# Performance work log

Measured on AMD Instinct MI355X. Metric: run time of the kernel, lower is better.

Reference implementation:

```python
import jax, jax.numpy as jnp
import numpy as np

NUM_NODES = 50000
NUM_RELATIONS = 16
HIDDEN = 128
NUM_LAYERS = 3
NUM_EDGES = 1600000


def setup_inputs() -> dict:
    key = jax.random.key(0)
    ks = jax.random.split(key, 6)
    edge_index = jax.random.randint(ks[0], (2, NUM_EDGES), 0, NUM_NODES, dtype=jnp.int64)
    edge_type = jax.random.randint(ks[1], (NUM_EDGES,), 0, NUM_RELATIONS, dtype=jnp.int64)
    scale = 1.0 / np.sqrt(HIDDEN)
    node_init = jax.random.normal(ks[2], (NUM_NODES, HIDDEN), dtype=jnp.float32) * scale
    W = jax.random.normal(ks[3], (NUM_LAYERS, NUM_RELATIONS, HIDDEN, HIDDEN), dtype=jnp.float32) * scale
    root = jax.random.normal(ks[4], (NUM_LAYERS, HIDDEN, HIDDEN), dtype=jnp.float32) * scale
    bias = jnp.zeros((NUM_LAYERS, HIDDEN), dtype=jnp.float32)
    return {"edge_index": edge_index, "edge_type": edge_type,
            "node_init": node_init, "W": W, "root": root, "bias": bias}


def _fast_rgcn_layer(x, src, tgt, edge_type, W_r, root_r, bias_r):
    # FastRGCNConv with aggr='mean': mean of messages per (target node, relation),
    # message = x_src @ W[relation]. By linearity, aggregate normalized x_src per
    # (node, relation) first, then apply relation weights with a single einsum.
    N, d = x.shape
    R = W_r.shape[0]
    seg = tgt * R + edge_type                       # combined (node, relation) segment id
    msg = x[src]                                    # [E, d] irregular gather
    agg = jax.ops.segment_sum(msg, seg, num_segments=N * R).reshape(N, R, d)
    cnt = jax.ops.segment_sum(jnp.ones_like(edge_type, dtype=x.dtype), seg,
                              num_segments=N * R).reshape(N, R, 1)
    agg = agg / jnp.clip(cnt, 1.0, None)            # per-(node,relation) mean
    out = jnp.einsum('nrd,rdo->no', agg, W_r)       # relation-specific transform
    out = out + x @ root_r + bias_r                 # root/self connection + bias
    return out


def reference(edge_index, edge_type, node_init, W, root, bias):
    src, tgt = edge_index[0], edge_index[1]
    x = node_init
    for i in range(NUM_LAYERS):
        x = _fast_rgcn_layer(x, src, tgt, edge_type, W[i], root[i], bias[i])
        if i < NUM_LAYERS - 1:
            x = jax.nn.relu(x)  # dropout omitted (eval mode)
    return x
```

## Files before the change

### kernel.cpp

```cpp
#include <hip/hip_runtime.h>
#include <hip/hip_bf16.h>

#define N_NODES   50000
#define N_REL     16
#define HID       128
#define N_EDGES   1600000
#define N_TILES   3125
#define N_BINS    800000
#define N_RUNS    50000
#define N_SCANBLK 49
#define N_MBLK    1563
#define PAYLOAD_CAP 2400064
#define BS_LAYER  278528
#define AG_STRIDE 136

typedef unsigned short ushort_t;
typedef __attribute__((ext_vector_type(8))) short short8;
typedef __attribute__((ext_vector_type(4))) float f32x4;

union BF2U { __hip_bfloat162 h; unsigned u; };

__device__ __forceinline__ unsigned pack_bf16_2(float x, float y) {
  BF2U c; c.h = __float22bfloat162_rn(make_float2(x, y));
  return c.u;
}

__device__ __forceinline__ void lds_barrier() {
  asm volatile("s_waitcnt lgkmcnt(0)\n\ts_barrier" ::: "memory");
}


__global__ __launch_bounds__(256) void k_hist(const int* __restrict__ ei,
                                              const int* __restrict__ et,
                                              int* __restrict__ cnt,
                                              int* __restrict__ rank) {
  int e = blockIdx.x * 256 + threadIdx.x;
  int tgt = ei[N_EDGES + e];
  int r   = et[e];
  int key = ((tgt >> 4) << 8) | (r << 4) | (tgt & 15);
  rank[e] = atomicAdd(&cnt[key], 1);
}

__global__ __launch_bounds__(1024) void k_runpad_btot(const int* __restrict__ cnt,
                                                      int* __restrict__ run_start,
                                                      int* __restrict__ totals) {
  __shared__ int s[1024];
  int t = threadIdx.x, blk = blockIdx.x;
  int r = blk * 1024 + t;
  int v = 0;
  if (r < N_RUNS) {
    const int4* c4 = (const int4*)(cnt + r * 16);
    int sum = 0;
#pragma unroll
    for (int j = 0; j < 4; ++j) { int4 w = c4[j]; sum += w.x + w.y + w.z + w.w; }
    v = (sum + 15) & ~15;
    run_start[r] = v;
  }
  s[t] = v; __syncthreads();
  for (int ofs = 512; ofs > 0; ofs >>= 1) {
    if (t < ofs) s[t] += s[t + ofs];
    __syncthreads();
  }
  if (t == 0) totals[blk] = s[0];
}

__global__ __launch_bounds__(1024) void k_scan_totals(int* totals, int* endp, int nblk) {
  __shared__ int s[1024];
  int t = threadIdx.x;
  int v = (t < nblk) ? totals[t] : 0;
  s[t] = v; __syncthreads();
  for (int ofs = 1; ofs < 1024; ofs <<= 1) {
    int x = (t >= ofs) ? s[t - ofs] : 0;
    __syncthreads();
    s[t] += x;
    __syncthreads();
  }
  if (t < nblk) totals[t] = s[t] - v;
  if (t == nblk - 1) *endp = s[t];
}

__global__ __launch_bounds__(1024) void k_scan_fineoff(int* __restrict__ run_start,
                                                       const int* __restrict__ totals,
                                                       const int* __restrict__ cnt,
                                                       int* __restrict__ fine_start,
                                                       unsigned* __restrict__ payload) {
  __shared__ int s[1024];
  int t = threadIdx.x, blk = blockIdx.x;
  int r = blk * 1024 + t;
  int v = (r < N_RUNS) ? run_start[r] : 0;
  s[t] = v; __syncthreads();
  for (int ofs = 1; ofs < 1024; ofs <<= 1) {
    int x = (t >= ofs) ? s[t - ofs] : 0;
    __syncthreads();
    s[t] += x;
    __syncthreads();
  }
  if (r < N_RUNS) {
    int base = totals[blk] + s[t] - v;
    run_start[r] = base;
    int pfx = 0;
#pragma unroll 4
    for (int i = 0; i < 16; ++i) {
      fine_start[r * 16 + i] = base + pfx;
      pfx += cnt[r * 16 + i];
    }
    const unsigned dummy = ((unsigned)N_NODES << 16) | (1u << 4) | 15u;
    for (int j = base + pfx; j < base + v; ++j) payload[j] = dummy;
  }
}

__global__ __launch_bounds__(256) void k_sort(const int* __restrict__ ei,
                                              const int* __restrict__ et,
                                              const int* __restrict__ cnt,
                                              const int* __restrict__ fine_start,
                                              const int* __restrict__ rank,
                                              unsigned* __restrict__ payload) {
  int e = blockIdx.x * 256 + threadIdx.x;
  int src = ei[e];
  int tgt = ei[N_EDGES + e];
  int r   = et[e];
  int key = ((tgt >> 4) << 8) | (r << 4) | (tgt & 15);
  int c = cnt[key]; c = c > 4095 ? 4095 : c;
  int pos = fine_start[key] + rank[e];
  payload[pos] = ((unsigned)src << 16) | ((unsigned)c << 4) | (unsigned)(tgt & 15);
}

__global__ __launch_bounds__(256) void k_bt(const float* __restrict__ W,
                                            const float* __restrict__ root,
                                            ushort_t* __restrict__ Bs) {
  int idx = blockIdx.x * 256 + threadIdx.x;
  int lane = idx & 63;
  int fl   = idx >> 6;
  int frag = fl % 544;
  int l    = fl / 544;
  int cb = frag & 7, kk = (frag >> 3) & 3, r = frag >> 5;
  int col = cb * 16 + (lane & 15);
  int d0  = kk * 32 + (lane >> 4) * 8;
  const float* srcp = (r < 16)
      ? W + ((size_t)(l * N_REL + r) * HID + d0) * HID + col
      : root + ((size_t)l * HID + d0) * HID + col;
  ushort_t out[8];
#pragma unroll
  for (int j = 0; j < 8; ++j) {
    union { __hip_bfloat16 h; ushort_t u; } c;
    c.h = __float2bfloat16(srcp[(size_t)j * HID]);
    out[j] = c.u;
  }
  *(short8*)(Bs + ((size_t)fl << 9) + lane * 8) = *(short8*)out;
}

__global__ __launch_bounds__(256) void k_xh(const float* __restrict__ xin,
                                            ushort_t* __restrict__ xh_a,
                                            ushort_t* __restrict__ xh_b) {
  int i = blockIdx.x * 256 + threadIdx.x;
  float4 v = ((const float4*)xin)[i];
  uint2 u;
  u.x = pack_bf16_2(v.x, v.y);
  u.y = pack_bf16_2(v.z, v.w);
  ((uint2*)xh_a)[i] = u;
  if (blockIdx.x == 0 && threadIdx.x < 64) {
    uint2 z = {0u, 0u};
    ushort_t* dst = (threadIdx.x < 32) ? xh_a : xh_b;
    int k = threadIdx.x & 31;
    *(uint2*)(dst + (size_t)N_NODES * HID + k * 4) = z;
  }
}


__global__ __launch_bounds__(512, 8) void k_main(const ushort_t* __restrict__ xh,
                                                 ushort_t* __restrict__ xh_out,
                                                 float* __restrict__ fout,
                                                 const ushort_t* __restrict__ Bs,
                                                 const float* __restrict__ bias,
                                                 const int* __restrict__ run_start,
                                                 const unsigned* __restrict__ payload,
                                                 int write_f32) {
  __shared__ alignas(16) ushort_t agg[2][2][32][AG_STRIDE];

  const int tile0 = blockIdx.x * 2;
  const int tid   = threadIdx.x;
  const int wave  = tid >> 6;
  const int lane  = tid & 63;
  const int m16   = lane & 15;
  const int q     = lane >> 4;
  const unsigned* xh32 = (const unsigned*)xh;

  if (wave < 4) {
    const int p_rel  = wave & 1;
    const int p_tile = wave >> 1;
    const int rowb   = p_tile * 16;

    int ebv = 0;
    {
      int tt = tile0 + p_tile;
      int idx = (tt < N_TILES) ? (tt * 16 + (lane >> 1) * 2 + p_rel + (lane & 1))
                               : N_RUNS;
      if (lane < 16) ebv = run_start[idx];
    }

#define ISSUE16(DST, PV, JB)                                                  \
    _Pragma("unroll")                                                         \
    for (int k1 = 0; k1 < 16; ++k1) {                                         \
      unsigned spq = (unsigned)__builtin_amdgcn_readlane(PV, (JB) + k1);      \
      DST[k1] = xh32[(spq >> 16) * 64 + lane];                                \
    }

#define FLUSHM(BUF)                                                           \
    if (mcur >= 0) {                                                          \
      float sc = __builtin_amdgcn_rcpf((float)scnt);                          \
      *(unsigned*)&agg[BUF][p_rel][rowb + mcur][lane * 2] =                   \
          pack_bf16_2(a0 * sc, a1 * sc);                                      \
    }

#define CONSUME1(SPK, XV, BUF)                                                \
    {                                                                         \
      int mk = (int)((SPK) & 15u);                                            \
      if (mk != mcur) {                                                       \
        FLUSHM(BUF);                                                          \
        mcur = mk; scnt = (int)(((SPK) >> 4) & 4095u);                        \
        a0 = 0.f; a1 = 0.f;                                                   \
      }                                                                       \
      a0 += __uint_as_float((XV) << 16);                                      \
      a1 += __uint_as_float((XV) & 0xffff0000u);                              \
    }

#define CONS16(PV, JB, SLOT, BUF)                                             \
    _Pragma("unroll")                                                         \
    for (int k2 = 0; k2 < 16; ++k2) {                                         \
      unsigned spk = (unsigned)__builtin_amdgcn_readlane(PV, (JB) + k2);      \
      CONSUME1(spk, SLOT[k2], BUF);                                           \
    }

    unsigned xqA[16], xqB[16], xqE[16];

    int e0 = __builtin_amdgcn_readlane(ebv, 0);
    int e1 = __builtin_amdgcn_readlane(ebv, 1);
    int pv = (int)payload[e0 + lane];
    ISSUE16(xqA, pv, 0);

    for (int s = 0; s < 8; ++s) {
      const int buf = s & 1;
      int cnt = e1 - e0;

      if (cnt > 16) ISSUE16(xqB, pv, 16);
      if (cnt > 32) ISSUE16(xqE, pv, 32);

      int f0 = e0, f1 = e1, pvn = pv;
      if (s < 7) {
        f0 = __builtin_amdgcn_readlane(ebv, (s + 1) * 2);
        f1 = __builtin_amdgcn_readlane(ebv, (s + 1) * 2 + 1);
        pvn = (int)payload[f0 + lane];
      }

      {
        short8 z = {0, 0, 0, 0, 0, 0, 0, 0};
#pragma unroll
        for (int i = 0; i < 4; ++i)
          *(short8*)&agg[buf][p_rel][rowb + i * 4 + q][m16 * 8] = z;
      }

      {
        int mcur = -1, scnt = 1;
        float a0 = 0.f, a1 = 0.f;
        if (cnt > 0) {
          CONS16(pv, 0, xqA, buf);
          if (cnt > 16) {
            CONS16(pv, 16, xqB, buf);
            if (cnt > 32) {
              CONS16(pv, 32, xqE, buf);
              if (cnt > 48) {
                ISSUE16(xqB, pv, 48);
                CONS16(pv, 48, xqB, buf);
              }
            }
          }
          for (int c0 = e0 + 64; c0 < e1; c0 += 16) {
            int pvx = (int)payload[c0 + lane];
            ISSUE16(xqE, pvx, 0);
            CONS16(pvx, 0, xqE, buf);
          }
          FLUSHM(buf);
        }
      }

      if (s < 7) {
        e0 = f0; e1 = f1; pv = pvn;
        ISSUE16(xqA, pv, 0);
      }
      lds_barrier();
    }
#undef CONS16
#undef CONSUME1
#undef FLUSHM
#undef ISSUE16
    return;
  }

  const int cw = wave - 4;
  f32x4 acc[2][2];
#pragma unroll
  for (int t = 0; t < 2; ++t)
#pragma unroll
    for (int i = 0; i < 2; ++i) acc[t][i] = (f32x4){0.f, 0.f, 0.f, 0.f};

  for (int s = 0; s < 8; ++s) {
    lds_barrier();
#pragma unroll
    for (int rp = 0; rp < 2; ++rp) {
      int rel = s * 2 + rp;
      short8 Bf[4][2];
#pragma unroll
      for (int kk = 0; kk < 4; ++kk)
#pragma unroll
        for (int i = 0; i < 2; ++i)
          Bf[kk][i] = *(const short8*)(Bs +
              ((size_t)((rel * 4 + kk) * 8 + (cw * 2 + i)) << 9) + lane * 8);
#pragma unroll
      for (int kk = 0; kk < 4; ++kk) {
        short8 A0 = *(const short8*)&agg[s & 1][rp][m16][kk * 32 + q * 8];
        short8 A1 = *(const short8*)&agg[s & 1][rp][16 + m16][kk * 32 + q * 8];
#pragma unroll
        for (int i = 0; i < 2; ++i) {
          acc[0][i] = __builtin_amdgcn_mfma_f32_16x16x32_bf16(A0, Bf[kk][i], acc[0][i], 0, 0, 0);
          acc[1][i] = __builtin_amdgcn_mfma_f32_16x16x32_bf16(A1, Bf[kk][i], acc[1][i], 0, 0, 0);
        }
      }
    }
  }

  {
    short8 Bf[4][2];
#pragma unroll
    for (int kk = 0; kk < 4; ++kk)
#pragma unroll
      for (int i = 0; i < 2; ++i)
        Bf[kk][i] = *(const short8*)(Bs +
            ((size_t)((16 * 4 + kk) * 8 + (cw * 2 + i)) << 9) + lane * 8);
    int r0 = tile0 * 16 + m16;      if (r0 > N_NODES) r0 = N_NODES;
    int r1 = tile0 * 16 + 16 + m16; if (r1 > N_NODES) r1 = N_NODES;
#pragma unroll
    for (int kk = 0; kk < 4; ++kk) {
      short8 A0 = *(const short8*)(xh + (size_t)r0 * HID + kk * 32 + q * 8);
      short8 A1 = *(const short8*)(xh + (size_t)r1 * HID + kk * 32 + q * 8);
#pragma unroll
      for (int i = 0; i < 2; ++i) {
        acc[0][i] = __builtin_amdgcn_mfma_f32_16x16x32_bf16(A0, Bf[kk][i], acc[0][i], 0, 0, 0);
        acc[1][i] = __builtin_amdgcn_mfma_f32_16x16x32_bf16(A1, Bf[kk][i], acc[1][i], 0, 0, 0);
      }
    }
  }

  float bvv[2];
#pragma unroll
  for (int i = 0; i < 2; ++i) bvv[i] = bias[cw * 32 + i * 16 + m16];
  int rbase = tile0 * 16 + q * 4;
#pragma unroll
  for (int t = 0; t < 2; ++t)
#pragma unroll
    for (int rg = 0; rg < 4; ++rg) {
      int row = rbase + t * 16 + rg;
      if (row < N_NODES) {
#pragma unroll
        for (int i = 0; i < 2; ++i) {
          float v = acc[t][i][rg] + bvv[i];
          int col = cw * 32 + i * 16 + m16;
          if (write_f32) {
            fout[(size_t)row * HID + col] = v;
          } else {
            v = fmaxf(v, 0.f);
            union { __hip_bfloat16 h; ushort_t u; } cv;
            cv.h = __float2bfloat16(v);
            xh_out[(size_t)row * HID + col] = cv.u;
          }
        }
      }
    }
}


extern "C" void kernel_launch(void* const* d_in, const int* in_sizes, int n_in,
                              void* d_out, int out_size, void* d_ws, size_t ws_size,
                              hipStream_t stream) {
  const int*   ei        = (const int*)d_in[0];
  const int*   et        = (const int*)d_in[1];
  const float* node_init = (const float*)d_in[2];
  const float* W         = (const float*)d_in[3];
  const float* root      = (const float*)d_in[4];
  const float* bias      = (const float*)d_in[5];
  float* outp = (float*)d_out;

  char* ws = (char*)d_ws;
  size_t o = 0;
  auto carve = [&](size_t bytes) { char* p = ws + o; o = (o + bytes + 255) & ~(size_t)255; return p; };
  ushort_t* xh_a       = (ushort_t*)carve((size_t)(N_NODES + 1) * HID * 2);
  ushort_t* xh_b       = (ushort_t*)carve((size_t)(N_NODES + 1) * HID * 2);
  unsigned* payload    = (unsigned*)carve((size_t)PAYLOAD_CAP * 4);
  int*      cnt        = (int*)     carve((size_t)N_BINS * 4);
  int*      fine_start = (int*)     carve((size_t)N_BINS * 4);
  int*      rank       = (int*)     carve((size_t)N_EDGES * 4);
  int*      run_start  = (int*)     carve((size_t)(N_RUNS + 1) * 4);
  int*      totals     = (int*)     carve((size_t)N_SCANBLK * 4);
  ushort_t* Bs         = (ushort_t*)carve((size_t)3 * BS_LAYER * 2);
  (void)ws_size; (void)n_in; (void)in_sizes; (void)out_size;

  hipMemsetAsync(cnt, 0, (size_t)N_BINS * 4, stream);
  hipLaunchKernelGGL(k_hist,         dim3(N_EDGES / 256), dim3(256), 0, stream, ei, et, cnt, rank);
  hipLaunchKernelGGL(k_runpad_btot,  dim3(N_SCANBLK), dim3(1024), 0, stream, cnt, run_start, totals);
  hipLaunchKernelGGL(k_scan_totals,  dim3(1), dim3(1024), 0, stream, totals, run_start + N_RUNS, N_SCANBLK);
  hipLaunchKernelGGL(k_scan_fineoff, dim3(N_SCANBLK), dim3(1024), 0, stream, run_start, totals, cnt, fine_start, payload);
  hipLaunchKernelGGL(k_sort,         dim3(N_EDGES / 256), dim3(256), 0, stream, ei, et, cnt, fine_start, rank, payload);
  hipLaunchKernelGGL(k_bt,           dim3(3 * 544 * 64 / 256), dim3(256), 0, stream, W, root, Bs);
  hipLaunchKernelGGL(k_xh,           dim3(N_NODES * HID / 4 / 256), dim3(256), 0, stream, node_init, xh_a, xh_b);

  hipLaunchKernelGGL(k_main, dim3(N_MBLK), dim3(512), 0, stream,
                     xh_a, xh_b, (float*)nullptr,
                     Bs + (size_t)0 * BS_LAYER, bias + 0 * HID, run_start, payload, 0);
  hipLaunchKernelGGL(k_main, dim3(N_MBLK), dim3(512), 0, stream,
                     xh_b, xh_a, (float*)nullptr,
                     Bs + (size_t)1 * BS_LAYER, bias + 1 * HID, run_start, payload, 0);
  hipLaunchKernelGGL(k_main, dim3(N_MBLK), dim3(512), 0, stream,
                     xh_a, (ushort_t*)nullptr, outp,
                     Bs + (size_t)2 * BS_LAYER, bias + 2 * HID, run_start, payload, 1);
}
```

Baseline: 509.0 us.

## Collapse preprocessing kernels: single-pass scan with atomic cursor, packed key-rank, fused conversions

Replaces the three-kernel run/fine-offset scan with one kernel. Each block takes its base offset from an atomic cursor and stores a (base, count) pair per run, which the main kernel now reads. The histogram pass writes a packed key|rank word so the sort pass no longer re-reads target and edge-type arrays. The weight-transpose and feature bf16 conversion kernels are merged into one launch. The aim is fewer launches and serialization points plus less global traffic in preprocessing, at the cost of run placement order depending on block scheduling and an assumption that per-bin ranks fit in 12 bits.

```diff
diff --git a/kernel.cpp b/kernel.cpp
--- a/kernel.cpp
+++ b/kernel.cpp
@@ -13,6 +13,8 @@
 #define PAYLOAD_CAP 2400064
 #define BS_LAYER  278528
 #define AG_STRIDE 136
+#define XH_BLKS   6250
+#define BT_BLKS   408
 
 typedef unsigned short ushort_t;
 typedef __attribute__((ext_vector_type(8))) short short8;
@@ -33,41 +35,33 @@
 __global__ __launch_bounds__(256) void k_hist(const int* __restrict__ ei,
                                               const int* __restrict__ et,
                                               int* __restrict__ cnt,
-                                              int* __restrict__ rank) {
+                                              unsigned* __restrict__ keyrank) {
   int e = blockIdx.x * 256 + threadIdx.x;
   int tgt = ei[N_EDGES + e];
   int r   = et[e];
   int key = ((tgt >> 4) << 8) | (r << 4) | (tgt & 15);
-  rank[e] = atomicAdd(&cnt[key], 1);
-}
-
-__global__ __launch_bounds__(1024) void k_runpad_btot(const int* __restrict__ cnt,
-                                                      int* __restrict__ run_start,
-                                                      int* __restrict__ totals) {
+  int rk  = atomicAdd(&cnt[key], 1);
+  keyrank[e] = ((unsigned)key << 12) | (unsigned)rk;
+}
+
+__global__ __launch_bounds__(1024) void k_scanall(const int* __restrict__ cnt,
+                                                  int* __restrict__ run2,
+                                                  int* __restrict__ fine_start,
+                                                  unsigned* __restrict__ payload,
+                                                  int* __restrict__ cursor) {
   __shared__ int s[1024];
+  __shared__ int basesh;
   int t = threadIdx.x, blk = blockIdx.x;
   int r = blk * 1024 + t;
+  int4 c4[4];
   int v = 0;
   if (r < N_RUNS) {
-    const int4* c4 = (const int4*)(cnt + r * 16);
+    const int4* cp = (const int4*)(cnt + r * 16);
     int sum = 0;
 #pragma unroll
-    for (int j = 0; j < 4; ++j) { int4 w = c4[j]; sum += w.x + w.y + w.z + w.w; }
+    for (int j = 0; j < 4; ++j) { c4[j] = cp[j]; sum += c4[j].x + c4[j].y + c4[j].z + c4[j].w; }
     v = (sum + 15) & ~15;
-    run_start[r] = v;
-  }
-  s[t] = v; __syncthreads();
-  for (int ofs = 512; ofs > 0; ofs >>= 1) {
-    if (t < ofs) s[t] += s[t + ofs];
-    __syncthreads();
-  }
-  if (t == 0) totals[blk] = s[0];
-}
-
-__global__ __launch_bounds__(1024) void k_scan_totals(int* totals, int* endp, int nblk) {
-  __shared__ int s[1024];
-  int t = threadIdx.x;
-  int v = (t < nblk) ? totals[t] : 0;
+  }
   s[t] = v; __syncthreads();
   for (int ofs = 1; ofs < 1024; ofs <<= 1) {
     int x = (t >= ofs) ? s[t - ofs] : 0;
@@ -75,34 +69,22 @@
     s[t] += x;
     __syncthreads();
   }
-  if (t < nblk) totals[t] = s[t] - v;
-  if (t == nblk - 1) *endp = s[t];
-}
-
-__global__ __launch_bounds__(1024) void k_scan_fineoff(int* __restrict__ run_start,
-                                                       const int* __restrict__ totals,
-                                                       const int* __restrict__ cnt,
-                                                       int* __restrict__ fine_start,
-                                                       unsigned* __restrict__ payload) {
-  __shared__ int s[1024];
-  int t = threadIdx.x, blk = blockIdx.x;
-  int r = blk * 1024 + t;
-  int v = (r < N_RUNS) ? run_start[r] : 0;
-  s[t] = v; __syncthreads();
-  for (int ofs = 1; ofs < 1024; ofs <<= 1) {
-    int x = (t >= ofs) ? s[t - ofs] : 0;
-    __syncthreads();
-    s[t] += x;
-    __syncthreads();
-  }
+  if (t == 1023) basesh = atomicAdd(cursor, s[1023]);
+  __syncthreads();
   if (r < N_RUNS) {
-    int base = totals[blk] + s[t] - v;
-    run_start[r] = base;
+    int base = basesh + s[t] - v;
+    run2[r * 2]     = base;
+    run2[r * 2 + 1] = v;
+    int c16[16];
+    c16[0]=c4[0].x; c16[1]=c4[0].y; c16[2]=c4[0].z; c16[3]=c4[0].w;
+    c16[4]=c4[1].x; c16[5]=c4[1].y; c16[6]=c4[1].z; c16[7]=c4[1].w;
+    c16[8]=c4[2].x; c16[9]=c4[2].y; c16[10]=c4[2].z; c16[11]=c4[2].w;
+    c16[12]=c4[3].x; c16[13]=c4[3].y; c16[14]=c4[3].z; c16[15]=c4[3].w;
     int pfx = 0;
-#pragma unroll 4
+#pragma unroll
     for (int i = 0; i < 16; ++i) {
       fine_start[r * 16 + i] = base + pfx;
-      pfx += cnt[r * 16 + i];
+      pfx += c16[i];
     }
     const unsigned dummy = ((unsigned)N_NODES << 16) | (1u << 4) | 15u;
     for (int j = base + pfx; j < base + v; ++j) payload[j] = dummy;
@@ -110,25 +92,42 @@
 }
 
 __global__ __launch_bounds__(256) void k_sort(const int* __restrict__ ei,
-                                              const int* __restrict__ et,
                                               const int* __restrict__ cnt,
                                               const int* __restrict__ fine_start,
-                                              const int* __restrict__ rank,
+                                              const unsigned* __restrict__ keyrank,
                                               unsigned* __restrict__ payload) {
   int e = blockIdx.x * 256 + threadIdx.x;
   int src = ei[e];
-  int tgt = ei[N_EDGES + e];
-  int r   = et[e];
-  int key = ((tgt >> 4) << 8) | (r << 4) | (tgt & 15);
+  unsigned kr = keyrank[e];
+  int key = (int)(kr >> 12);
+  int rk  = (int)(kr & 4095u);
   int c = cnt[key]; c = c > 4095 ? 4095 : c;
-  int pos = fine_start[key] + rank[e];
-  payload[pos] = ((unsigned)src << 16) | ((unsigned)c << 4) | (unsigned)(tgt & 15);
-}
-
-__global__ __launch_bounds__(256) void k_bt(const float* __restrict__ W,
-                                            const float* __restrict__ root,
-                                            ushort_t* __restrict__ Bs) {
-  int idx = blockIdx.x * 256 + threadIdx.x;
+  int pos = fine_start[key] + rk;
+  payload[pos] = ((unsigned)src << 16) | ((unsigned)c << 4) | (unsigned)(key & 15);
+}
+
+__global__ __launch_bounds__(256) void k_btxh(const float* __restrict__ W,
+                                              const float* __restrict__ root,
+                                              ushort_t* __restrict__ Bs,
+                                              const float* __restrict__ xin,
+                                              ushort_t* __restrict__ xh_a,
+                                              ushort_t* __restrict__ xh_b) {
+  if (blockIdx.x < XH_BLKS) {
+    int i = blockIdx.x * 256 + threadIdx.x;
+    float4 v = ((const float4*)xin)[i];
+    uint2 u;
+    u.x = pack_bf16_2(v.x, v.y);
+    u.y = pack_bf16_2(v.z, v.w);
+    ((uint2*)xh_a)[i] = u;
+    if (blockIdx.x == 0 && threadIdx.x < 64) {
+      uint2 z = {0u, 0u};
+      ushort_t* dst = (threadIdx.x < 32) ? xh_a : xh_b;
+      int k = threadIdx.x & 31;
+      *(uint2*)(dst + (size_t)N_NODES * HID + k * 4) = z;
+    }
+    return;
+  }
+  int idx = (blockIdx.x - XH_BLKS) * 256 + threadIdx.x;
   int lane = idx & 63;
   int fl   = idx >> 6;
   int frag = fl % 544;
@@ -149,30 +148,13 @@
   *(short8*)(Bs + ((size_t)fl << 9) + lane * 8) = *(short8*)out;
 }
 
-__global__ __launch_bounds__(256) void k_xh(const float* __restrict__ xin,
-                                            ushort_t* __restrict__ xh_a,
-                                            ushort_t* __restrict__ xh_b) {
-  int i = blockIdx.x * 256 + threadIdx.x;
-  float4 v = ((const float4*)xin)[i];
-  uint2 u;
-  u.x = pack_bf16_2(v.x, v.y);
-  u.y = pack_bf16_2(v.z, v.w);
-  ((uint2*)xh_a)[i] = u;
-  if (blockIdx.x == 0 && threadIdx.x < 64) {
-    uint2 z = {0u, 0u};
-    ushort_t* dst = (threadIdx.x < 32) ? xh_a : xh_b;
-    int k = threadIdx.x & 31;
-    *(uint2*)(dst + (size_t)N_NODES * HID + k * 4) = z;
-  }
-}
-
 
 __global__ __launch_bounds__(512, 8) void k_main(const ushort_t* __restrict__ xh,
                                                  ushort_t* __restrict__ xh_out,
                                                  float* __restrict__ fout,
                                                  const ushort_t* __restrict__ Bs,
                                                  const float* __restrict__ bias,
-                                                 const int* __restrict__ run_start,
+                                                 const int* __restrict__ run2,
                                                  const unsigned* __restrict__ payload,
                                                  int write_f32) {
   __shared__ alignas(16) ushort_t agg[2][2][32][AG_STRIDE];
@@ -193,9 +175,10 @@
     int ebv = 0;
     {
       int tt = tile0 + p_tile;
-      int idx = (tt < N_TILES) ? (tt * 16 + (lane >> 1) * 2 + p_rel + (lane & 1))
-                               : N_RUNS;
-      if (lane < 16) ebv = run_start[idx];
+      if (lane < 16 && tt < N_TILES) {
+        int rid = tt * 16 + ((lane >> 1) << 1) + p_rel;
+        ebv = run2[rid * 2 + (lane & 1)];
+      }
     }
 
 #define ISSUE16(DST, PV, JB)                                                  \
@@ -233,22 +216,22 @@
 
     unsigned xqA[16], xqB[16], xqE[16];
 
-    int e0 = __builtin_amdgcn_readlane(ebv, 0);
-    int e1 = __builtin_amdgcn_readlane(ebv, 1);
+    int e0   = __builtin_amdgcn_readlane(ebv, 0);
+    int rcnt = __builtin_amdgcn_readlane(ebv, 1);
     int pv = (int)payload[e0 + lane];
     ISSUE16(xqA, pv, 0);
 
     for (int s = 0; s < 8; ++s) {
       const int buf = s & 1;
-      int cnt = e1 - e0;
+      int cnt = rcnt;
 
       if (cnt > 16) ISSUE16(xqB, pv, 16);
       if (cnt > 32) ISSUE16(xqE, pv, 32);
 
-      int f0 = e0, f1 = e1, pvn = pv;
+      int f0 = e0, fcnt = rcnt, pvn = pv;
       if (s < 7) {
-        f0 = __builtin_amdgcn_readlane(ebv, (s + 1) * 2);
-        f1 = __builtin_amdgcn_readlane(ebv, (s + 1) * 2 + 1);
+        f0   = __builtin_amdgcn_readlane(ebv, (s + 1) * 2);
+        fcnt = __builtin_amdgcn_readlane(ebv, (s + 1) * 2 + 1);
         pvn = (int)payload[f0 + lane];
       }
 
@@ -274,7 +257,7 @@
               }
             }
           }
-          for (int c0 = e0 + 64; c0 < e1; c0 += 16) {
+          for (int c0 = e0 + 64; c0 < e0 + cnt; c0 += 16) {
             int pvx = (int)payload[c0 + lane];
             ISSUE16(xqE, pvx, 0);
             CONS16(pvx, 0, xqE, buf);
@@ -284,7 +267,7 @@
       }
 
       if (s < 7) {
-        e0 = f0; e1 = f1; pv = pvn;
+        e0 = f0; rcnt = fcnt; pv = pvn;
         ISSUE16(xqA, pv, 0);
       }
       lds_barrier();
@@ -395,30 +378,27 @@
   ushort_t* xh_a       = (ushort_t*)carve((size_t)(N_NODES + 1) * HID * 2);
   ushort_t* xh_b       = (ushort_t*)carve((size_t)(N_NODES + 1) * HID * 2);
   unsigned* payload    = (unsigned*)carve((size_t)PAYLOAD_CAP * 4);
-  int*      cnt        = (int*)     carve((size_t)N_BINS * 4);
+  int*      cnt        = (int*)     carve((size_t)(N_BINS + 64) * 4);
   int*      fine_start = (int*)     carve((size_t)N_BINS * 4);
-  int*      rank       = (int*)     carve((size_t)N_EDGES * 4);
-  int*      run_start  = (int*)     carve((size_t)(N_RUNS + 1) * 4);
-  int*      totals     = (int*)     carve((size_t)N_SCANBLK * 4);
+  unsigned* keyrank    = (unsigned*)carve((size_t)N_EDGES * 4);
+  int*      run2       = (int*)     carve((size_t)(N_RUNS * 2 + 2) * 4);
   ushort_t* Bs         = (ushort_t*)carve((size_t)3 * BS_LAYER * 2);
+  int*      cursor     = cnt + N_BINS;
   (void)ws_size; (void)n_in; (void)in_sizes; (void)out_size;
 
-  hipMemsetAsync(cnt, 0, (size_t)N_BINS * 4, stream);
-  hipLaunchKernelGGL(k_hist,         dim3(N_EDGES / 256), dim3(256), 0, stream, ei, et, cnt, rank);
-  hipLaunchKernelGGL(k_runpad_btot,  dim3(N_SCANBLK), dim3(1024), 0, stream, cnt, run_start, totals);
-  hipLaunchKernelGGL(k_scan_totals,  dim3(1), dim3(1024), 0, stream, totals, run_start + N_RUNS, N_SCANBLK);
-  hipLaunchKernelGGL(k_scan_fineoff, dim3(N_SCANBLK), dim3(1024), 0, stream, run_start, totals, cnt, fine_start, payload);
-  hipLaunchKernelGGL(k_sort,         dim3(N_EDGES / 256), dim3(256), 0, stream, ei, et, cnt, fine_start, rank, payload);
-  hipLaunchKernelGGL(k_bt,           dim3(3 * 544 * 64 / 256), dim3(256), 0, stream, W, root, Bs);
-  hipLaunchKernelGGL(k_xh,           dim3(N_NODES * HID / 4 / 256), dim3(256), 0, stream, node_init, xh_a, xh_b);
+  hipMemsetAsync(cnt, 0, (size_t)(N_BINS + 64) * 4, stream);
+  hipLaunchKernelGGL(k_hist,    dim3(N_EDGES / 256), dim3(256), 0, stream, ei, et, cnt, keyrank);
+  hipLaunchKernelGGL(k_scanall, dim3(N_SCANBLK), dim3(1024), 0, stream, cnt, run2, fine_start, payload, cursor);
+  hipLaunchKernelGGL(k_sort,    dim3(N_EDGES / 256), dim3(256), 0, stream, ei, cnt, fine_start, keyrank, payload);
+  hipLaunchKernelGGL(k_btxh,    dim3(XH_BLKS + BT_BLKS), dim3(256), 0, stream, W, root, Bs, node_init, xh_a, xh_b);
 
   hipLaunchKernelGGL(k_main, dim3(N_MBLK), dim3(512), 0, stream,
                      xh_a, xh_b, (float*)nullptr,
-                     Bs + (size_t)0 * BS_LAYER, bias + 0 * HID, run_start, payload, 0);
+                     Bs + (size_t)0 * BS_LAYER, bias + 0 * HID, run2, payload, 0);
   hipLaunchKernelGGL(k_main, dim3(N_MBLK), dim3(512), 0, stream,
                      xh_b, xh_a, (float*)nullptr,
-                     Bs + (size_t)1 * BS_LAYER, bias + 1 * HID, run_start, payload, 0);
+                     Bs + (size_t)1 * BS_LAYER, bias + 1 * HID, run2, payload, 0);
   hipLaunchKernelGGL(k_main, dim3(N_MBLK), dim3(512), 0, stream,
                      xh_a, (ushort_t*)nullptr, outp,
-                     Bs + (size_t)2 * BS_LAYER, bias + 2 * HID, run_start, payload, 1);
-}
+                     Bs + (size_t)2 * BS_LAYER, bias + 2 * HID, run2, payload, 1);
+}
```

Result: faster. 496.1 us (-2.5%).
